# Kernel optimization log

Hardware: AMD Instinct MI355X
Metric: run time of the kernel (lower is better)

The kernel has to match this reference:

```python
import jax, jax.numpy as jnp
import numpy as np

EMB = 768
HEADS = 12
HEAD_DIM = EMB // HEADS


def setup_inputs() -> dict:
    key = jax.random.key(0)
    k1, k2, k3, k4 = jax.random.split(key, 4)
    x = jax.random.normal(k1, (8, 1024, EMB), dtype=jnp.float32)
    # Dense kernels, TF default glorot-ish scale approximated with small normals
    w_qkv = jax.random.normal(k2, (EMB, 3 * EMB), dtype=jnp.float32) * 0.02
    w_out = jax.random.normal(k3, (EMB, EMB), dtype=jnp.float32) * 0.02
    b_out = jnp.zeros((EMB,), dtype=jnp.float32)
    return {"x": x, "w_qkv": w_qkv, "w_out": w_out, "b_out": b_out}


def reference(x, w_qkv, w_out, b_out):
    B, S, E = x.shape
    qkv = jnp.einsum("bse,ef->bsf", x, w_qkv)                 # [B,S,3E]
    qkv = qkv.reshape(B, S, 3, HEADS, HEAD_DIM)
    qkv = jnp.transpose(qkv, (2, 0, 3, 1, 4))                  # [3,B,H,S,D]
    q, k, v = qkv[0], qkv[1], qkv[2]
    scale = jnp.float32(HEAD_DIM) ** -0.5
    # Blocked loop in source computes exact full (non-causal) attention:
    # every query block attends to all keys -> equivalent to standard SDPA.
    scores = jnp.einsum("bhqd,bhkd->bhqk", q, k) * scale       # [B,H,S,S]
    probs = jax.nn.softmax(scores, axis=-1)
    out = jnp.einsum("bhqk,bhkd->bhqd", probs, v)              # [B,H,S,D]
    out = jnp.transpose(out, (0, 2, 1, 3)).reshape(B, S, E)
    return jnp.einsum("bse,ef->bsf", out, w_out) + b_out
```

## Files before the change

kernel.cpp:

```cpp
#include <hip/hip_runtime.h>

typedef float f32x4 __attribute__((ext_vector_type(4)));
typedef short bf16x8 __attribute__((ext_vector_type(8)));

#define MFMA_BF16(a, b, c) __builtin_amdgcn_mfma_f32_16x16x32_bf16((a), (b), (c), 0, 0, 0)

#define GLDS16(gp, lp) __builtin_amdgcn_global_load_lds( \
    (const __attribute__((address_space(1))) unsigned int*)(gp), \
    (__attribute__((address_space(3))) unsigned int*)(lp), 16, 0, 0)

__device__ __forceinline__ ushort f2bf(float f) {
    unsigned int u = __float_as_uint(f);
    return (ushort)((u + 0x7FFFu + ((u >> 16) & 1u)) >> 16);
}

__device__ __forceinline__ float fexp2(float x) {
#if __has_builtin(__builtin_amdgcn_exp2f)
    return __builtin_amdgcn_exp2f(x);
#else
    return exp2f(x);
#endif
}

__global__ __launch_bounds__(256) void prep_kernel(
    const float* __restrict__ x, const float* __restrict__ wq, const float* __restrict__ wo,
    ushort* __restrict__ xb, ushort* __restrict__ wqbt, ushort* __restrict__ wobt)
{
    __shared__ float tile[32][33];
    const int bid = blockIdx.x;
    if (bid < 2048) {
        const float4* src = (const float4*)x;
        ushort4* dst = (ushort4*)xb;
        for (int i = bid * 256 + threadIdx.x; i < 1572864; i += 2048 * 256) {
            float4 v = src[i];
            ushort4 o;
            o.x = f2bf(v.x); o.y = f2bf(v.y); o.z = f2bf(v.z); o.w = f2bf(v.w);
            dst[i] = o;
        }
        return;
    }
    const float* src; ushort* dst; int K, N, bx, by;
    if (bid < 3776) {
        const int L = bid - 2048;
        src = wq; dst = wqbt; K = 768; N = 2304; bx = L % 72; by = L / 72;
    } else {
        const int L = bid - 3776;
        src = wo; dst = wobt; K = 768; N = 768; bx = L % 24; by = L / 24;
    }
    const int n0 = bx * 32, k0 = by * 32;
    const int c = threadIdx.x & 31, rb = threadIdx.x >> 5;
    #pragma unroll
    for (int i = 0; i < 4; ++i)
        tile[i * 8 + rb][c] = src[(size_t)(k0 + i * 8 + rb) * N + n0 + c];
    __syncthreads();
    #pragma unroll
    for (int i = 0; i < 4; ++i) {
        int nr = i * 8 + rb;
        dst[(size_t)(n0 + nr) * K + k0 + c] = f2bf(tile[c][nr]);
    }
}

__global__ __launch_bounds__(256) void gemm_qkv_mfma(
    const ushort* __restrict__ A, const ushort* __restrict__ Bt,
    ushort* __restrict__ Qo, ushort* __restrict__ Ko, ushort* __restrict__ Vo)
{
    __shared__ ushort Al[2][8192];
    __shared__ ushort Bl[2][8192];
    const int tid = threadIdx.x, lane = tid & 63;
    const int wv = tid >> 6, lo = lane & 15, hi = lane >> 4;
    const int wr = wv >> 1, wc = wv & 1;
    const int L = blockIdx.x;
    const int nid = (L & 7) * 144 + (L >> 3);
    const int n0 = (nid % 18) * 128, m0 = (nid / 18) * 128;

    auto stage = [&](int bi, int k0) {
        #pragma unroll
        for (int it = 0; it < 4; ++it) {
            const int p = it * 256 + tid;
            const int row = p >> 3, ch = (p & 7) ^ (row & 7);
            GLDS16(A + (size_t)(m0 + row) * 768 + k0 + ch * 8,
                   &Al[bi][(it * 256 + (tid & 192)) * 8]);
        }
        #pragma unroll
        for (int it = 0; it < 4; ++it) {
            const int p = it * 256 + tid;
            const int row = p >> 3, ch = (p & 7) ^ (row & 7);
            GLDS16(Bt + (size_t)(n0 + row) * 768 + k0 + ch * 8,
                   &Bl[bi][(it * 256 + (tid & 192)) * 8]);
        }
    };

    f32x4 acc[4][4];
    #pragma unroll
    for (int i = 0; i < 4; ++i)
        #pragma unroll
        for (int j = 0; j < 4; ++j)
            acc[i][j] = (f32x4){0.f, 0.f, 0.f, 0.f};

    const int region = n0 / 768;
    const int h = ((n0 % 768) >> 6) + wc;

    stage(0, 0);
    stage(1, 64);

    int cur = 0;
    for (int t = 0; t < 12; ++t) {
        if (t < 11) asm volatile("s_waitcnt vmcnt(8)" ::: "memory");
        else        asm volatile("s_waitcnt vmcnt(0)" ::: "memory");
        __builtin_amdgcn_s_barrier();
        asm volatile("" ::: "memory");

        #pragma unroll
        for (int ks = 0; ks < 2; ++ks) {
            bf16x8 af[4], bfr[4];
            #pragma unroll
            for (int i = 0; i < 4; ++i) {
                const int ra = wr * 64 + i * 16 + lo;
                af[i] = *(const bf16x8*)&Al[cur][ra * 64 + (((ks * 4 + hi) ^ (ra & 7)) * 8)];
                const int rb = wc * 64 + i * 16 + lo;
                bfr[i] = *(const bf16x8*)&Bl[cur][rb * 64 + (((ks * 4 + hi) ^ (rb & 7)) * 8)];
            }
            if (region == 2) {
                #pragma unroll
                for (int mi = 0; mi < 4; ++mi)
                    #pragma unroll
                    for (int nj = 0; nj < 4; ++nj)
                        acc[mi][nj] = MFMA_BF16(af[mi], bfr[nj], acc[mi][nj]);
            } else {
                #pragma unroll
                for (int mi = 0; mi < 4; ++mi)
                    #pragma unroll
                    for (int nj = 0; nj < 4; ++nj)
                        acc[mi][nj] = MFMA_BF16(bfr[nj], af[mi], acc[mi][nj]);
            }
        }

        asm volatile("s_waitcnt lgkmcnt(0)" ::: "memory");
        __builtin_amdgcn_s_barrier();
        asm volatile("" ::: "memory");
        if (t + 2 < 12) stage(cur, (t + 2) * 64);
        cur ^= 1;
    }

    if (region == 2) {
        #pragma unroll
        for (int mi = 0; mi < 4; ++mi) {
            const int m4 = m0 + wr * 64 + mi * 16 + hi * 4;
            const int b = m4 >> 10, s = m4 & 1023;
            #pragma unroll
            for (int nj = 0; nj < 4; ++nj) {
                const int d = nj * 16 + lo;
                ushort4 pk;
                pk.x = f2bf(acc[mi][nj][0]); pk.y = f2bf(acc[mi][nj][1]);
                pk.z = f2bf(acc[mi][nj][2]); pk.w = f2bf(acc[mi][nj][3]);
                *(ushort4*)&Vo[((size_t)(b * 12 + h) * 64 + d) * 1024 + s] = pk;
            }
        }
    } else {
        ushort* dst = region ? Ko : Qo;
        const float sc = region ? 1.0f : 0.18033688011112042f;
        #pragma unroll
        for (int mi = 0; mi < 4; ++mi) {
            const int s_idx = m0 + wr * 64 + mi * 16 + lo;
            const int b = s_idx >> 10, s = s_idx & 1023;
            const size_t base = ((size_t)(b * 12 + h) * 1024 + s) * 64;
            #pragma unroll
            for (int nj = 0; nj < 4; ++nj) {
                ushort4 pk;
                pk.x = f2bf(acc[mi][nj][0] * sc); pk.y = f2bf(acc[mi][nj][1] * sc);
                pk.z = f2bf(acc[mi][nj][2] * sc); pk.w = f2bf(acc[mi][nj][3] * sc);
                *(ushort4*)&dst[base + nj * 16 + hi * 4] = pk;
            }
        }
    }
}

__global__ __launch_bounds__(256) void attn_mfma_kernel(
    const ushort* __restrict__ Qg, const ushort* __restrict__ Kg,
    const ushort* __restrict__ Vg, ushort* __restrict__ AO)
{
    __shared__ ushort Kl[2][4096];
    __shared__ ushort Vl[2][4096];
    __shared__ ushort Pl[4][32 * 72];

    const int tid = threadIdx.x, lane = tid & 63;
    const int wv = tid >> 6, lo = lane & 15, hi = lane >> 4;
    const int L = blockIdx.x;
    const int xcd = L & 7, g = L >> 3;
    const int qb = g / 12;
    const int bh = xcd * 12 + (g % 12);
    const int b = bh / 12, h = bh % 12;
    const size_t kvbase = (size_t)bh * (1024 * 64);

    bf16x8 qa[2][2];
    const int qrow0 = qb * 128 + wv * 32;
    #pragma unroll
    for (int mi = 0; mi < 2; ++mi)
        #pragma unroll
        for (int ks = 0; ks < 2; ++ks)
            qa[mi][ks] = *(const bf16x8*)&Qg[kvbase + (size_t)(qrow0 + mi * 16 + lo) * 64 + ks * 32 + hi * 8];

    f32x4 o[2][4];
    float lp[2] = {0.f, 0.f};
    #pragma unroll
    for (int mi = 0; mi < 2; ++mi)
        #pragma unroll
        for (int dj = 0; dj < 4; ++dj) o[mi][dj] = (f32x4){0.f, 0.f, 0.f, 0.f};

    auto stage = [&](int bi, int kt) {
        #pragma unroll
        for (int it = 0; it < 2; ++it) {
            const int p = it * 256 + tid;
            const int row = p >> 3, ch = (p & 7) ^ (row & 7);
            GLDS16(Kg + kvbase + (size_t)(kt + row) * 64 + ch * 8, &Kl[bi][(it * 256 + (tid & 192)) * 8]);
        }
        #pragma unroll
        for (int it = 0; it < 2; ++it) {
            const int p = it * 256 + tid;
            const int row = p >> 3, ch = (p & 7) ^ (row & 7);
            GLDS16(Vg + kvbase + (size_t)row * 1024 + kt + ch * 8, &Vl[bi][(it * 256 + (tid & 192)) * 8]);
        }
    };

    stage(0, 0);
    __syncthreads();

    for (int t = 0; t < 16; ++t) {
        const int cur = t & 1;
        if (t < 15) stage(cur ^ 1, (t + 1) * 64);

        f32x4 s[2][4];
        #pragma unroll
        for (int mi = 0; mi < 2; ++mi)
            #pragma unroll
            for (int nj = 0; nj < 4; ++nj) s[mi][nj] = (f32x4){0.f, 0.f, 0.f, 0.f};
        #pragma unroll
        for (int ks = 0; ks < 2; ++ks) {
            bf16x8 kb[4];
            #pragma unroll
            for (int nj = 0; nj < 4; ++nj) {
                const int key = nj * 16 + lo, c = ks * 4 + hi;
                kb[nj] = *(const bf16x8*)&Kl[cur][key * 64 + ((c ^ (key & 7)) * 8)];
            }
            #pragma unroll
            for (int mi = 0; mi < 2; ++mi)
                #pragma unroll
                for (int nj = 0; nj < 4; ++nj)
                    s[mi][nj] = MFMA_BF16(kb[nj], qa[mi][ks], s[mi][nj]);
        }

        #pragma unroll
        for (int mi = 0; mi < 2; ++mi) {
            #pragma unroll
            for (int nj = 0; nj < 4; ++nj) {
                const unsigned int u0 = __float_as_uint(fexp2(s[mi][nj][0]));
                const unsigned int u1 = __float_as_uint(fexp2(s[mi][nj][1]));
                const unsigned int u2 = __float_as_uint(fexp2(s[mi][nj][2]));
                const unsigned int u3 = __float_as_uint(fexp2(s[mi][nj][3]));
                const float t0 = __uint_as_float(u0 & 0xFFFF0000u);
                const float t1 = __uint_as_float(u1 & 0xFFFF0000u);
                const float t2 = __uint_as_float(u2 & 0xFFFF0000u);
                const float t3 = __uint_as_float(u3 & 0xFFFF0000u);
                lp[mi] += (t0 + t1) + (t2 + t3);
                ushort4 pk;
                pk.x = (ushort)(u0 >> 16); pk.y = (ushort)(u1 >> 16);
                pk.z = (ushort)(u2 >> 16); pk.w = (ushort)(u3 >> 16);
                *(ushort4*)&Pl[wv][(mi * 16 + lo) * 72 + nj * 16 + hi * 4] = pk;
            }
        }

        #pragma unroll
        for (int ks = 0; ks < 2; ++ks) {
            bf16x8 pa[2];
            #pragma unroll
            for (int mi = 0; mi < 2; ++mi)
                pa[mi] = *(const bf16x8*)&Pl[wv][(mi * 16 + lo) * 72 + ks * 32 + hi * 8];
            bf16x8 vb[4];
            #pragma unroll
            for (int dj = 0; dj < 4; ++dj) {
                const int d = dj * 16 + lo, c = ks * 4 + hi;
                vb[dj] = *(const bf16x8*)&Vl[cur][d * 64 + ((c ^ (d & 7)) * 8)];
            }
            #pragma unroll
            for (int mi = 0; mi < 2; ++mi)
                #pragma unroll
                for (int dj = 0; dj < 4; ++dj)
                    o[mi][dj] = MFMA_BF16(pa[mi], vb[dj], o[mi][dj]);
        }
        __syncthreads();
    }

    #pragma unroll
    for (int mi = 0; mi < 2; ++mi) {
        float l = lp[mi];
        l += __shfl_xor(l, 16);
        l += __shfl_xor(l, 32);
        #pragma unroll
        for (int r = 0; r < 4; ++r) {
            const float lr = __shfl(l, hi * 4 + r, 16);
            const float rcp = 1.0f / lr;
            const int srow = qrow0 + mi * 16 + hi * 4 + r;
            #pragma unroll
            for (int dj = 0; dj < 4; ++dj)
                AO[((size_t)(b * 1024 + srow)) * 768 + h * 64 + dj * 16 + lo] =
                    f2bf(o[mi][dj][r] * rcp);
        }
    }
}

__global__ __launch_bounds__(256) void gemm_out_mfma(
    const ushort* __restrict__ A, const ushort* __restrict__ Bt,
    const float* __restrict__ bias, float* __restrict__ C)
{
    __shared__ ushort Al[2][8192];
    __shared__ ushort Bl[2][8192];
    const int tid = threadIdx.x, lane = tid & 63;
    const int wv = tid >> 6, lo = lane & 15, hi = lane >> 4;
    const int wr = wv >> 1, wc = wv & 1;
    const int L = blockIdx.x;
    const int nid = (L & 7) * 48 + (L >> 3);
    const int n0 = (nid % 6) * 128, m0 = (nid / 6) * 128;

    auto stage = [&](int bi, int k0) {
        #pragma unroll
        for (int it = 0; it < 4; ++it) {
            const int p = it * 256 + tid;
            const int row = p >> 3, ch = (p & 7) ^ (row & 7);
            GLDS16(A + (size_t)(m0 + row) * 768 + k0 + ch * 8,
                   &Al[bi][(it * 256 + (tid & 192)) * 8]);
        }
        #pragma unroll
        for (int it = 0; it < 4; ++it) {
            const int p = it * 256 + tid;
            const int row = p >> 3, ch = (p & 7) ^ (row & 7);
            GLDS16(Bt + (size_t)(n0 + row) * 768 + k0 + ch * 8,
                   &Bl[bi][(it * 256 + (tid & 192)) * 8]);
        }
    };

    f32x4 acc[4][4];
    #pragma unroll
    for (int i = 0; i < 4; ++i)
        #pragma unroll
        for (int j = 0; j < 4; ++j)
            acc[i][j] = (f32x4){0.f, 0.f, 0.f, 0.f};

    stage(0, 0);
    stage(1, 64);

    int cur = 0;
    for (int t = 0; t < 12; ++t) {
        if (t < 11) asm volatile("s_waitcnt vmcnt(8)" ::: "memory");
        else        asm volatile("s_waitcnt vmcnt(0)" ::: "memory");
        __builtin_amdgcn_s_barrier();
        asm volatile("" ::: "memory");

        #pragma unroll
        for (int ks = 0; ks < 2; ++ks) {
            bf16x8 af[4], bfr[4];
            #pragma unroll
            for (int i = 0; i < 4; ++i) {
                const int ra = wr * 64 + i * 16 + lo;
                af[i] = *(const bf16x8*)&Al[cur][ra * 64 + (((ks * 4 + hi) ^ (ra & 7)) * 8)];
                const int rb = wc * 64 + i * 16 + lo;
                bfr[i] = *(const bf16x8*)&Bl[cur][rb * 64 + (((ks * 4 + hi) ^ (rb & 7)) * 8)];
            }
            #pragma unroll
            for (int mi = 0; mi < 4; ++mi)
                #pragma unroll
                for (int nj = 0; nj < 4; ++nj)
                    acc[mi][nj] = MFMA_BF16(bfr[nj], af[mi], acc[mi][nj]);
        }

        asm volatile("s_waitcnt lgkmcnt(0)" ::: "memory");
        __builtin_amdgcn_s_barrier();
        asm volatile("" ::: "memory");
        if (t + 2 < 12) stage(cur, (t + 2) * 64);
        cur ^= 1;
    }

    const int ncol0 = n0 + wc * 64;
    #pragma unroll
    for (int mi = 0; mi < 4; ++mi) {
        const int m = m0 + wr * 64 + mi * 16 + lo;
        #pragma unroll
        for (int nj = 0; nj < 4; ++nj) {
            const int nb = ncol0 + nj * 16 + hi * 4;
            const float4 bv = *reinterpret_cast<const float4*>(&bias[nb]);
            float4 ov;
            ov.x = acc[mi][nj][0] + bv.x; ov.y = acc[mi][nj][1] + bv.y;
            ov.z = acc[mi][nj][2] + bv.z; ov.w = acc[mi][nj][3] + bv.w;
            *reinterpret_cast<float4*>(&C[(size_t)m * 768 + nb]) = ov;
        }
    }
}

extern "C" void kernel_launch(void* const* d_in, const int* in_sizes, int n_in,
                              void* d_out, int out_size, void* d_ws, size_t ws_size,
                              hipStream_t stream) {
    const float* x     = (const float*)d_in[0];
    const float* w_qkv = (const float*)d_in[1];
    const float* w_out = (const float*)d_in[2];
    const float* b_out = (const float*)d_in[3];
    float* out = (float*)d_out;

    (void)in_sizes; (void)n_in; (void)out_size; (void)ws_size;

    ushort* xb   = (ushort*)d_ws;
    ushort* wqbt = xb + 6291456;
    ushort* wobt = wqbt + 1769472;
    ushort* Qs   = wobt + 589824;
    ushort* Ks   = Qs + 6291456;
    ushort* Vt   = Ks + 6291456;
    ushort* AO   = Vt + 6291456;

    prep_kernel<<<4352, 256, 0, stream>>>(x, w_qkv, w_out, xb, wqbt, wobt);
    gemm_qkv_mfma<<<1152, 256, 0, stream>>>(xb, wqbt, Qs, Ks, Vt);
    attn_mfma_kernel<<<768, 256, 0, stream>>>(Qs, Ks, Vt, AO);
    gemm_out_mfma<<<384, 256, 0, stream>>>(AO, wobt, b_out, out);
}
```

Measured before the change: 122.9 us.

## Fuse x fp32-to-bf16 conversion into QKV GEMM loads and raise MFMA priority

The separate pass that converts x to bf16 is removed. The QKV GEMM now streams fp32 x tiles straight into LDS and converts them to bf16 in registers with packed cvt instructions. To keep the LDS footprint the same, the K-tile is halved to 32, so there are twice as many pipeline iterations and barriers. The attention kernel also wraps its MFMA blocks in s_setprio so matrix work is favoured over other waves. This saves writing and re-reading a 12MB intermediate, but doubles the fp32 A traffic into LDS and adds barrier overhead.

```diff
diff --git a/kernel.cpp b/kernel.cpp
--- a/kernel.cpp
+++ b/kernel.cpp
@@ -22,29 +22,26 @@
 #endif
 }
 
+__device__ __forceinline__ bf16x8 cvt8(f32x4 a, f32x4 b) {
+    union { bf16x8 v; unsigned int u[4]; } r;
+    asm("v_cvt_pk_bf16_f32 %0, %1, %2" : "=v"(r.u[0]) : "v"(a[0]), "v"(a[1]));
+    asm("v_cvt_pk_bf16_f32 %0, %1, %2" : "=v"(r.u[1]) : "v"(a[2]), "v"(a[3]));
+    asm("v_cvt_pk_bf16_f32 %0, %1, %2" : "=v"(r.u[2]) : "v"(b[0]), "v"(b[1]));
+    asm("v_cvt_pk_bf16_f32 %0, %1, %2" : "=v"(r.u[3]) : "v"(b[2]), "v"(b[3]));
+    return r.v;
+}
+
 __global__ __launch_bounds__(256) void prep_kernel(
-    const float* __restrict__ x, const float* __restrict__ wq, const float* __restrict__ wo,
-    ushort* __restrict__ xb, ushort* __restrict__ wqbt, ushort* __restrict__ wobt)
+    const float* __restrict__ wq, const float* __restrict__ wo,
+    ushort* __restrict__ wqbt, ushort* __restrict__ wobt)
 {
     __shared__ float tile[32][33];
     const int bid = blockIdx.x;
-    if (bid < 2048) {
-        const float4* src = (const float4*)x;
-        ushort4* dst = (ushort4*)xb;
-        for (int i = bid * 256 + threadIdx.x; i < 1572864; i += 2048 * 256) {
-            float4 v = src[i];
-            ushort4 o;
-            o.x = f2bf(v.x); o.y = f2bf(v.y); o.z = f2bf(v.z); o.w = f2bf(v.w);
-            dst[i] = o;
-        }
-        return;
-    }
     const float* src; ushort* dst; int K, N, bx, by;
-    if (bid < 3776) {
-        const int L = bid - 2048;
-        src = wq; dst = wqbt; K = 768; N = 2304; bx = L % 72; by = L / 72;
+    if (bid < 1728) {
+        src = wq; dst = wqbt; K = 768; N = 2304; bx = bid % 72; by = bid / 72;
     } else {
-        const int L = bid - 3776;
+        const int L = bid - 1728;
         src = wo; dst = wobt; K = 768; N = 768; bx = L % 24; by = L / 24;
     }
     const int n0 = bx * 32, k0 = by * 32;
@@ -61,11 +58,11 @@
 }
 
 __global__ __launch_bounds__(256) void gemm_qkv_mfma(
-    const ushort* __restrict__ A, const ushort* __restrict__ Bt,
+    const float* __restrict__ X, const ushort* __restrict__ Bt,
     ushort* __restrict__ Qo, ushort* __restrict__ Ko, ushort* __restrict__ Vo)
 {
-    __shared__ ushort Al[2][8192];
-    __shared__ ushort Bl[2][8192];
+    __shared__ float  Af[2][4096];
+    __shared__ ushort Bl[2][4096];
     const int tid = threadIdx.x, lane = tid & 63;
     const int wv = tid >> 6, lo = lane & 15, hi = lane >> 4;
     const int wr = wv >> 1, wc = wv & 1;
@@ -76,16 +73,16 @@
     auto stage = [&](int bi, int k0) {
         #pragma unroll
         for (int it = 0; it < 4; ++it) {
-            const int p = it * 256 + tid;
-            const int row = p >> 3, ch = (p & 7) ^ (row & 7);
-            GLDS16(A + (size_t)(m0 + row) * 768 + k0 + ch * 8,
-                   &Al[bi][(it * 256 + (tid & 192)) * 8]);
-        }
-        #pragma unroll
-        for (int it = 0; it < 4; ++it) {
-            const int p = it * 256 + tid;
-            const int row = p >> 3, ch = (p & 7) ^ (row & 7);
-            GLDS16(Bt + (size_t)(n0 + row) * 768 + k0 + ch * 8,
+            const int q = it * 256 + tid;
+            const int row = q >> 3, c = q & 7;
+            GLDS16(X + (size_t)(m0 + row) * 768 + k0 + ((c ^ (row & 7)) * 4),
+                   &Af[bi][(it * 256 + (tid & 192)) * 4]);
+        }
+        #pragma unroll
+        for (int it = 0; it < 2; ++it) {
+            const int q = it * 256 + tid;
+            const int row = q >> 2, c = q & 3;
+            GLDS16(Bt + (size_t)(n0 + row) * 768 + k0 + ((c ^ (row & 3)) * 8),
                    &Bl[bi][(it * 256 + (tid & 192)) * 8]);
         }
     };
@@ -101,44 +98,43 @@
     const int h = ((n0 % 768) >> 6) + wc;
 
     stage(0, 0);
-    stage(1, 64);
+    stage(1, 32);
 
     int cur = 0;
-    for (int t = 0; t < 12; ++t) {
-        if (t < 11) asm volatile("s_waitcnt vmcnt(8)" ::: "memory");
+    for (int t = 0; t < 24; ++t) {
+        if (t < 23) asm volatile("s_waitcnt vmcnt(6)" ::: "memory");
         else        asm volatile("s_waitcnt vmcnt(0)" ::: "memory");
         __builtin_amdgcn_s_barrier();
         asm volatile("" ::: "memory");
 
-        #pragma unroll
-        for (int ks = 0; ks < 2; ++ks) {
-            bf16x8 af[4], bfr[4];
-            #pragma unroll
-            for (int i = 0; i < 4; ++i) {
-                const int ra = wr * 64 + i * 16 + lo;
-                af[i] = *(const bf16x8*)&Al[cur][ra * 64 + (((ks * 4 + hi) ^ (ra & 7)) * 8)];
-                const int rb = wc * 64 + i * 16 + lo;
-                bfr[i] = *(const bf16x8*)&Bl[cur][rb * 64 + (((ks * 4 + hi) ^ (rb & 7)) * 8)];
-            }
-            if (region == 2) {
+        bf16x8 af[4], bfr[4];
+        #pragma unroll
+        for (int i = 0; i < 4; ++i) {
+            const int ra = wr * 64 + i * 16 + lo;
+            const f32x4 a0 = *(const f32x4*)&Af[cur][ra * 32 + (((2 * hi)     ^ (ra & 7)) * 4)];
+            const f32x4 a1 = *(const f32x4*)&Af[cur][ra * 32 + (((2 * hi + 1) ^ (ra & 7)) * 4)];
+            af[i] = cvt8(a0, a1);
+            const int rb = wc * 64 + i * 16 + lo;
+            bfr[i] = *(const bf16x8*)&Bl[cur][rb * 32 + ((hi ^ (rb & 3)) * 8)];
+        }
+        if (region == 2) {
+            #pragma unroll
+            for (int mi = 0; mi < 4; ++mi)
                 #pragma unroll
-                for (int mi = 0; mi < 4; ++mi)
-                    #pragma unroll
-                    for (int nj = 0; nj < 4; ++nj)
-                        acc[mi][nj] = MFMA_BF16(af[mi], bfr[nj], acc[mi][nj]);
-            } else {
+                for (int nj = 0; nj < 4; ++nj)
+                    acc[mi][nj] = MFMA_BF16(af[mi], bfr[nj], acc[mi][nj]);
+        } else {
+            #pragma unroll
+            for (int mi = 0; mi < 4; ++mi)
                 #pragma unroll
-                for (int mi = 0; mi < 4; ++mi)
-                    #pragma unroll
-                    for (int nj = 0; nj < 4; ++nj)
-                        acc[mi][nj] = MFMA_BF16(bfr[nj], af[mi], acc[mi][nj]);
-            }
+                for (int nj = 0; nj < 4; ++nj)
+                    acc[mi][nj] = MFMA_BF16(bfr[nj], af[mi], acc[mi][nj]);
         }
 
         asm volatile("s_waitcnt lgkmcnt(0)" ::: "memory");
         __builtin_amdgcn_s_barrier();
         asm volatile("" ::: "memory");
-        if (t + 2 < 12) stage(cur, (t + 2) * 64);
+        if (t + 2 < 24) stage(cur, (t + 2) * 32);
         cur ^= 1;
     }
 
@@ -242,11 +238,13 @@
                 const int key = nj * 16 + lo, c = ks * 4 + hi;
                 kb[nj] = *(const bf16x8*)&Kl[cur][key * 64 + ((c ^ (key & 7)) * 8)];
             }
+            __builtin_amdgcn_s_setprio(1);
             #pragma unroll
             for (int mi = 0; mi < 2; ++mi)
                 #pragma unroll
                 for (int nj = 0; nj < 4; ++nj)
                     s[mi][nj] = MFMA_BF16(kb[nj], qa[mi][ks], s[mi][nj]);
+            __builtin_amdgcn_s_setprio(0);
         }
 
         #pragma unroll
@@ -281,11 +279,13 @@
                 const int d = dj * 16 + lo, c = ks * 4 + hi;
                 vb[dj] = *(const bf16x8*)&Vl[cur][d * 64 + ((c ^ (d & 7)) * 8)];
             }
+            __builtin_amdgcn_s_setprio(1);
             #pragma unroll
             for (int mi = 0; mi < 2; ++mi)
                 #pragma unroll
                 for (int dj = 0; dj < 4; ++dj)
                     o[mi][dj] = MFMA_BF16(pa[mi], vb[dj], o[mi][dj]);
+            __builtin_amdgcn_s_setprio(0);
         }
         __syncthreads();
     }
@@ -406,16 +406,15 @@
 
     (void)in_sizes; (void)n_in; (void)out_size; (void)ws_size;
 
-    ushort* xb   = (ushort*)d_ws;
-    ushort* wqbt = xb + 6291456;
+    ushort* wqbt = (ushort*)d_ws;
     ushort* wobt = wqbt + 1769472;
     ushort* Qs   = wobt + 589824;
     ushort* Ks   = Qs + 6291456;
     ushort* Vt   = Ks + 6291456;
     ushort* AO   = Vt + 6291456;
 
-    prep_kernel<<<4352, 256, 0, stream>>>(x, w_qkv, w_out, xb, wqbt, wobt);
-    gemm_qkv_mfma<<<1152, 256, 0, stream>>>(xb, wqbt, Qs, Ks, Vt);
+    prep_kernel<<<2304, 256, 0, stream>>>(w_qkv, w_out, wqbt, wobt);
+    gemm_qkv_mfma<<<1152, 256, 0, stream>>>(x, wqbt, Qs, Ks, Vt);
     attn_mfma_kernel<<<768, 256, 0, stream>>>(Qs, Ks, Vt, AO);
     gemm_out_mfma<<<384, 256, 0, stream>>>(AO, wobt, b_out, out);
 }
```

Measured after the change: 139.1 us. 1.13x slower.

## Enlarge QKV GEMM tiles to 256x256 with 8 waves and staggered staging

Applied to the files above, without the earlier changes.

The QKV projection GEMM now uses 256x256 output tiles computed by 512-thread blocks (8 waves, 2x4 layout). Each wave holds a 128x64 accumulator, and the grid drops from 1152 to 288 blocks. Loads are interleaved in quarter-steps with barriers, B fragments are kept in registers per K-tile, and s_setprio raises MFMA priority. The attention kernel also gets s_setprio around its MFMA loops. The aim is higher data reuse and better overlap of loads with compute. The cost is more registers and LDS per block and fewer blocks, with 288 blocks on 256 CUs leaving a partial second wave.

```diff
diff --git a/kernel.cpp b/kernel.cpp
--- a/kernel.cpp
+++ b/kernel.cpp
@@ -60,92 +60,168 @@
     }
 }
 
-__global__ __launch_bounds__(256) void gemm_qkv_mfma(
+__global__ __launch_bounds__(512, 2) void gemm_qkv_mfma(
     const ushort* __restrict__ A, const ushort* __restrict__ Bt,
     ushort* __restrict__ Qo, ushort* __restrict__ Ko, ushort* __restrict__ Vo)
 {
-    __shared__ ushort Al[2][8192];
-    __shared__ ushort Bl[2][8192];
+    __shared__ ushort Abuf[2][16384];
+    __shared__ ushort Bbuf[2][16384];
     const int tid = threadIdx.x, lane = tid & 63;
     const int wv = tid >> 6, lo = lane & 15, hi = lane >> 4;
-    const int wr = wv >> 1, wc = wv & 1;
+    const int wr = wv >> 2, wc = wv & 3;
     const int L = blockIdx.x;
-    const int nid = (L & 7) * 144 + (L >> 3);
-    const int n0 = (nid % 18) * 128, m0 = (nid / 18) * 128;
-
-    auto stage = [&](int bi, int k0) {
-        #pragma unroll
-        for (int it = 0; it < 4; ++it) {
-            const int p = it * 256 + tid;
-            const int row = p >> 3, ch = (p & 7) ^ (row & 7);
-            GLDS16(A + (size_t)(m0 + row) * 768 + k0 + ch * 8,
-                   &Al[bi][(it * 256 + (tid & 192)) * 8]);
-        }
-        #pragma unroll
-        for (int it = 0; it < 4; ++it) {
-            const int p = it * 256 + tid;
-            const int row = p >> 3, ch = (p & 7) ^ (row & 7);
-            GLDS16(Bt + (size_t)(n0 + row) * 768 + k0 + ch * 8,
-                   &Bl[bi][(it * 256 + (tid & 192)) * 8]);
+    const int nid = (L & 7) * 36 + (L >> 3);
+    const int m0 = (nid / 9) * 256, n0 = (nid % 9) * 256;
+
+    const int region = n0 / 768;
+
+    auto stageA = [&](int bi, int half, int kt) {
+        #pragma unroll
+        for (int c = 0; c < 2; ++c) {
+            const int cl = c * 512 + tid;
+            const int row = half * 128 + (cl >> 3), sl = cl & 7;
+            GLDS16(A + (size_t)(m0 + row) * 768 + kt * 64 + ((sl ^ (row & 7)) * 8),
+                   &Abuf[bi][(half * 1024 + c * 512 + (tid & 448)) * 8]);
         }
     };
-
-    f32x4 acc[4][4];
-    #pragma unroll
-    for (int i = 0; i < 4; ++i)
+    auto stageB = [&](int bi, int half, int kt) {
+        #pragma unroll
+        for (int c = 0; c < 2; ++c) {
+            const int cl = c * 512 + tid;
+            const int row = half * 128 + (cl >> 3), sl = cl & 7;
+            GLDS16(Bt + (size_t)(n0 + row) * 768 + kt * 64 + ((sl ^ (row & 7)) * 8),
+                   &Bbuf[bi][(half * 1024 + c * 512 + (tid & 448)) * 8]);
+        }
+    };
+
+    f32x4 acc[8][4];
+    #pragma unroll
+    for (int i = 0; i < 8; ++i)
         #pragma unroll
         for (int j = 0; j < 4; ++j)
             acc[i][j] = (f32x4){0.f, 0.f, 0.f, 0.f};
 
-    const int region = n0 / 768;
-    const int h = ((n0 % 768) >> 6) + wc;
-
-    stage(0, 0);
-    stage(1, 64);
-
-    int cur = 0;
-    for (int t = 0; t < 12; ++t) {
-        if (t < 11) asm volatile("s_waitcnt vmcnt(8)" ::: "memory");
-        else        asm volatile("s_waitcnt vmcnt(0)" ::: "memory");
-        __builtin_amdgcn_s_barrier();
-        asm volatile("" ::: "memory");
-
-        #pragma unroll
-        for (int ks = 0; ks < 2; ++ks) {
-            bf16x8 af[4], bfr[4];
-            #pragma unroll
-            for (int i = 0; i < 4; ++i) {
-                const int ra = wr * 64 + i * 16 + lo;
-                af[i] = *(const bf16x8*)&Al[cur][ra * 64 + (((ks * 4 + hi) ^ (ra & 7)) * 8)];
-                const int rb = wc * 64 + i * 16 + lo;
-                bfr[i] = *(const bf16x8*)&Bl[cur][rb * 64 + (((ks * 4 + hi) ^ (rb & 7)) * 8)];
-            }
+    stageB(0, 0, 0); stageB(0, 1, 0);
+    stageA(0, 0, 0); stageA(0, 1, 0);
+    stageB(1, 0, 1); stageB(1, 1, 1);
+    asm volatile("s_waitcnt vmcnt(4)" ::: "memory");
+    __builtin_amdgcn_s_barrier();
+    asm volatile("" ::: "memory");
+
+    bf16x8 bfr[8];
+
+    for (int it = 0; it < 6; ++it) {
+        const int t1 = 2 * it + 1;
+        const int kB2 = (2 * it + 2) % 12;
+        const int kB3 = (2 * it + 3) % 12;
+
+        #pragma unroll
+        for (int q = 0; q < 4; ++q) {
+            if (q == 0) {
+                #pragma unroll
+                for (int nj = 0; nj < 4; ++nj)
+                    #pragma unroll
+                    for (int ks = 0; ks < 2; ++ks) {
+                        const int row = wc * 64 + nj * 16 + lo;
+                        bfr[nj * 2 + ks] = *(const bf16x8*)&Bbuf[0][row * 64 + (((ks * 4 + hi) ^ (row & 7)) * 8)];
+                    }
+            }
+            bf16x8 af[4];
+            #pragma unroll
+            for (int mm = 0; mm < 2; ++mm)
+                #pragma unroll
+                for (int ks = 0; ks < 2; ++ks) {
+                    const int row = wr * 128 + (2 * q + mm) * 16 + lo;
+                    af[mm * 2 + ks] = *(const bf16x8*)&Abuf[0][row * 64 + (((ks * 4 + hi) ^ (row & 7)) * 8)];
+                }
+            if (q == 0)      stageA(1, 0, t1);
+            else if (q == 1) stageA(1, 1, t1);
+            else if (q == 2) stageB(0, 0, kB2);
+            else             stageB(0, 1, kB2);
+            if (q == 0) asm volatile("s_waitcnt lgkmcnt(8)" ::: "memory");
+            __builtin_amdgcn_s_barrier();
+            asm volatile("s_waitcnt lgkmcnt(0)" ::: "memory");
+            __builtin_amdgcn_s_setprio(1);
             if (region == 2) {
                 #pragma unroll
-                for (int mi = 0; mi < 4; ++mi)
+                for (int mm = 0; mm < 2; ++mm)
                     #pragma unroll
                     for (int nj = 0; nj < 4; ++nj)
-                        acc[mi][nj] = MFMA_BF16(af[mi], bfr[nj], acc[mi][nj]);
+                        #pragma unroll
+                        for (int ks = 0; ks < 2; ++ks)
+                            acc[2 * q + mm][nj] = MFMA_BF16(af[mm * 2 + ks], bfr[nj * 2 + ks], acc[2 * q + mm][nj]);
             } else {
                 #pragma unroll
-                for (int mi = 0; mi < 4; ++mi)
+                for (int mm = 0; mm < 2; ++mm)
                     #pragma unroll
                     for (int nj = 0; nj < 4; ++nj)
-                        acc[mi][nj] = MFMA_BF16(bfr[nj], af[mi], acc[mi][nj]);
-            }
-        }
-
-        asm volatile("s_waitcnt lgkmcnt(0)" ::: "memory");
-        __builtin_amdgcn_s_barrier();
-        asm volatile("" ::: "memory");
-        if (t + 2 < 12) stage(cur, (t + 2) * 64);
-        cur ^= 1;
-    }
-
+                        #pragma unroll
+                        for (int ks = 0; ks < 2; ++ks)
+                            acc[2 * q + mm][nj] = MFMA_BF16(bfr[nj * 2 + ks], af[mm * 2 + ks], acc[2 * q + mm][nj]);
+            }
+            __builtin_amdgcn_s_setprio(0);
+            if (q == 3) asm volatile("s_waitcnt vmcnt(4)" ::: "memory");
+            __builtin_amdgcn_s_barrier();
+            asm volatile("" ::: "memory");
+        }
+
+        #pragma unroll
+        for (int q = 0; q < 4; ++q) {
+            if (q == 0) {
+                #pragma unroll
+                for (int nj = 0; nj < 4; ++nj)
+                    #pragma unroll
+                    for (int ks = 0; ks < 2; ++ks) {
+                        const int row = wc * 64 + nj * 16 + lo;
+                        bfr[nj * 2 + ks] = *(const bf16x8*)&Bbuf[1][row * 64 + (((ks * 4 + hi) ^ (row & 7)) * 8)];
+                    }
+            }
+            bf16x8 af[4];
+            #pragma unroll
+            for (int mm = 0; mm < 2; ++mm)
+                #pragma unroll
+                for (int ks = 0; ks < 2; ++ks) {
+                    const int row = wr * 128 + (2 * q + mm) * 16 + lo;
+                    af[mm * 2 + ks] = *(const bf16x8*)&Abuf[1][row * 64 + (((ks * 4 + hi) ^ (row & 7)) * 8)];
+                }
+            if (q == 0)      stageA(0, 0, kB2);
+            else if (q == 1) stageA(0, 1, kB2);
+            else if (q == 2) stageB(1, 0, kB3);
+            else             stageB(1, 1, kB3);
+            if (q == 0) asm volatile("s_waitcnt lgkmcnt(8)" ::: "memory");
+            __builtin_amdgcn_s_barrier();
+            asm volatile("s_waitcnt lgkmcnt(0)" ::: "memory");
+            __builtin_amdgcn_s_setprio(1);
+            if (region == 2) {
+                #pragma unroll
+                for (int mm = 0; mm < 2; ++mm)
+                    #pragma unroll
+                    for (int nj = 0; nj < 4; ++nj)
+                        #pragma unroll
+                        for (int ks = 0; ks < 2; ++ks)
+                            acc[2 * q + mm][nj] = MFMA_BF16(af[mm * 2 + ks], bfr[nj * 2 + ks], acc[2 * q + mm][nj]);
+            } else {
+                #pragma unroll
+                for (int mm = 0; mm < 2; ++mm)
+                    #pragma unroll
+                    for (int nj = 0; nj < 4; ++nj)
+                        #pragma unroll
+                        for (int ks = 0; ks < 2; ++ks)
+                            acc[2 * q + mm][nj] = MFMA_BF16(bfr[nj * 2 + ks], af[mm * 2 + ks], acc[2 * q + mm][nj]);
+            }
+            __builtin_amdgcn_s_setprio(0);
+            if (q == 3) asm volatile("s_waitcnt vmcnt(4)" ::: "memory");
+            __builtin_amdgcn_s_barrier();
+            asm volatile("" ::: "memory");
+        }
+    }
+    asm volatile("s_waitcnt vmcnt(0)" ::: "memory");
+
+    const int h = ((n0 + wc * 64) % 768) >> 6;
     if (region == 2) {
         #pragma unroll
-        for (int mi = 0; mi < 4; ++mi) {
-            const int m4 = m0 + wr * 64 + mi * 16 + hi * 4;
+        for (int mi = 0; mi < 8; ++mi) {
+            const int m4 = m0 + wr * 128 + mi * 16 + hi * 4;
             const int b = m4 >> 10, s = m4 & 1023;
             #pragma unroll
             for (int nj = 0; nj < 4; ++nj) {
@@ -160,8 +236,8 @@
         ushort* dst = region ? Ko : Qo;
         const float sc = region ? 1.0f : 0.18033688011112042f;
         #pragma unroll
-        for (int mi = 0; mi < 4; ++mi) {
-            const int s_idx = m0 + wr * 64 + mi * 16 + lo;
+        for (int mi = 0; mi < 8; ++mi) {
+            const int s_idx = m0 + wr * 128 + mi * 16 + lo;
             const int b = s_idx >> 10, s = s_idx & 1023;
             const size_t base = ((size_t)(b * 12 + h) * 1024 + s) * 64;
             #pragma unroll
@@ -242,11 +318,13 @@
                 const int key = nj * 16 + lo, c = ks * 4 + hi;
                 kb[nj] = *(const bf16x8*)&Kl[cur][key * 64 + ((c ^ (key & 7)) * 8)];
             }
+            __builtin_amdgcn_s_setprio(1);
             #pragma unroll
             for (int mi = 0; mi < 2; ++mi)
                 #pragma unroll
                 for (int nj = 0; nj < 4; ++nj)
                     s[mi][nj] = MFMA_BF16(kb[nj], qa[mi][ks], s[mi][nj]);
+            __builtin_amdgcn_s_setprio(0);
         }
 
         #pragma unroll
@@ -281,11 +359,13 @@
                 const int d = dj * 16 + lo, c = ks * 4 + hi;
                 vb[dj] = *(const bf16x8*)&Vl[cur][d * 64 + ((c ^ (d & 7)) * 8)];
             }
+            __builtin_amdgcn_s_setprio(1);
             #pragma unroll
             for (int mi = 0; mi < 2; ++mi)
                 #pragma unroll
                 for (int dj = 0; dj < 4; ++dj)
                     o[mi][dj] = MFMA_BF16(pa[mi], vb[dj], o[mi][dj]);
+            __builtin_amdgcn_s_setprio(0);
         }
         __syncthreads();
     }
@@ -415,7 +495,7 @@
     ushort* AO   = Vt + 6291456;
 
     prep_kernel<<<4352, 256, 0, stream>>>(x, w_qkv, w_out, xb, wqbt, wobt);
-    gemm_qkv_mfma<<<1152, 256, 0, stream>>>(xb, wqbt, Qs, Ks, Vt);
+    gemm_qkv_mfma<<<288, 512, 0, stream>>>(xb, wqbt, Qs, Ks, Vt);
     attn_mfma_kernel<<<768, 256, 0, stream>>>(Qs, Ks, Vt, AO);
     gemm_out_mfma<<<384, 256, 0, stream>>>(AO, wobt, b_out, out);
 }
```

Result: slower. 186.8 us (+52.1%).

## Make QKV GEMM persistent over three N-tiles per block; raise MFMA wave priority

Applied to the files above, without the earlier changes.

The QKV projection GEMM now launches 384 blocks, each handling three consecutive 128-column N-tiles for one M-tile. It streams 36 K-stages through a single continuous double-buffered pipeline and writes each tile's output when that tile finishes, instead of launching 1152 one-tile blocks. This removes the per-block prologue and tail, keeps the prefetch running across tile boundaries, and reuses the A rows that stay hot in cache. In exchange there is less parallelism (384 blocks against the CU count) and the epilogue stores now sit inside the loop. Separately, the attention kernel wraps its MFMA sequences in s_setprio so waves issuing matrix ops get scheduling priority.

```diff
diff --git a/kernel.cpp b/kernel.cpp
--- a/kernel.cpp
+++ b/kernel.cpp
@@ -70,10 +70,14 @@
     const int wv = tid >> 6, lo = lane & 15, hi = lane >> 4;
     const int wr = wv >> 1, wc = wv & 1;
     const int L = blockIdx.x;
-    const int nid = (L & 7) * 144 + (L >> 3);
-    const int n0 = (nid % 18) * 128, m0 = (nid / 18) * 128;
-
-    auto stage = [&](int bi, int k0) {
+    const int nid = (L & 7) * 48 + (L >> 3);
+    const int m0 = (nid / 6) * 128;
+    const int ngrp = nid % 6;
+    const int region = ngrp >> 1;
+
+    auto stage = [&](int bi, int s) {
+        const int k0 = (s % 12) * 64;
+        const int n0 = (ngrp * 3 + s / 12) * 128;
         #pragma unroll
         for (int it = 0; it < 4; ++it) {
             const int p = it * 256 + tid;
@@ -97,15 +101,12 @@
         for (int j = 0; j < 4; ++j)
             acc[i][j] = (f32x4){0.f, 0.f, 0.f, 0.f};
 
-    const int region = n0 / 768;
-    const int h = ((n0 % 768) >> 6) + wc;
-
     stage(0, 0);
-    stage(1, 64);
+    stage(1, 1);
 
     int cur = 0;
-    for (int t = 0; t < 12; ++t) {
-        if (t < 11) asm volatile("s_waitcnt vmcnt(8)" ::: "memory");
+    for (int s = 0; s < 36; ++s) {
+        if (s < 35) asm volatile("s_waitcnt vmcnt(8)" ::: "memory");
         else        asm volatile("s_waitcnt vmcnt(0)" ::: "memory");
         __builtin_amdgcn_s_barrier();
         asm volatile("" ::: "memory");
@@ -138,40 +139,50 @@
         asm volatile("s_waitcnt lgkmcnt(0)" ::: "memory");
         __builtin_amdgcn_s_barrier();
         asm volatile("" ::: "memory");
-        if (t + 2 < 12) stage(cur, (t + 2) * 64);
+
+        if ((s % 12) == 11) {
+            const int n0g = (ngrp * 3 + s / 12) * 128;
+            const int h = ((n0g % 768) >> 6) + wc;
+            if (region == 2) {
+                #pragma unroll
+                for (int mi = 0; mi < 4; ++mi) {
+                    const int m4 = m0 + wr * 64 + mi * 16 + hi * 4;
+                    const int b = m4 >> 10, sx = m4 & 1023;
+                    #pragma unroll
+                    for (int nj = 0; nj < 4; ++nj) {
+                        const int d = nj * 16 + lo;
+                        ushort4 pk;
+                        pk.x = f2bf(acc[mi][nj][0]); pk.y = f2bf(acc[mi][nj][1]);
+                        pk.z = f2bf(acc[mi][nj][2]); pk.w = f2bf(acc[mi][nj][3]);
+                        *(ushort4*)&Vo[((size_t)(b * 12 + h) * 64 + d) * 1024 + sx] = pk;
+                    }
+                }
+            } else {
+                ushort* dst = region ? Ko : Qo;
+                const float sc = region ? 1.0f : 0.18033688011112042f;
+                #pragma unroll
+                for (int mi = 0; mi < 4; ++mi) {
+                    const int s_idx = m0 + wr * 64 + mi * 16 + lo;
+                    const int b = s_idx >> 10, sx = s_idx & 1023;
+                    const size_t base = ((size_t)(b * 12 + h) * 1024 + sx) * 64;
+                    #pragma unroll
+                    for (int nj = 0; nj < 4; ++nj) {
+                        ushort4 pk;
+                        pk.x = f2bf(acc[mi][nj][0] * sc); pk.y = f2bf(acc[mi][nj][1] * sc);
+                        pk.z = f2bf(acc[mi][nj][2] * sc); pk.w = f2bf(acc[mi][nj][3] * sc);
+                        *(ushort4*)&dst[base + nj * 16 + hi * 4] = pk;
+                    }
+                }
+            }
+            #pragma unroll
+            for (int i = 0; i < 4; ++i)
+                #pragma unroll
+                for (int j = 0; j < 4; ++j)
+                    acc[i][j] = (f32x4){0.f, 0.f, 0.f, 0.f};
+        }
+
+        if (s + 2 < 36) stage(cur, s + 2);
         cur ^= 1;
-    }
-
-    if (region == 2) {
-        #pragma unroll
-        for (int mi = 0; mi < 4; ++mi) {
-            const int m4 = m0 + wr * 64 + mi * 16 + hi * 4;
-            const int b = m4 >> 10, s = m4 & 1023;
-            #pragma unroll
-            for (int nj = 0; nj < 4; ++nj) {
-                const int d = nj * 16 + lo;
-                ushort4 pk;
-                pk.x = f2bf(acc[mi][nj][0]); pk.y = f2bf(acc[mi][nj][1]);
-                pk.z = f2bf(acc[mi][nj][2]); pk.w = f2bf(acc[mi][nj][3]);
-                *(ushort4*)&Vo[((size_t)(b * 12 + h) * 64 + d) * 1024 + s] = pk;
-            }
-        }
-    } else {
-        ushort* dst = region ? Ko : Qo;
-        const float sc = region ? 1.0f : 0.18033688011112042f;
-        #pragma unroll
-        for (int mi = 0; mi < 4; ++mi) {
-            const int s_idx = m0 + wr * 64 + mi * 16 + lo;
-            const int b = s_idx >> 10, s = s_idx & 1023;
-            const size_t base = ((size_t)(b * 12 + h) * 1024 + s) * 64;
-            #pragma unroll
-            for (int nj = 0; nj < 4; ++nj) {
-                ushort4 pk;
-                pk.x = f2bf(acc[mi][nj][0] * sc); pk.y = f2bf(acc[mi][nj][1] * sc);
-                pk.z = f2bf(acc[mi][nj][2] * sc); pk.w = f2bf(acc[mi][nj][3] * sc);
-                *(ushort4*)&dst[base + nj * 16 + hi * 4] = pk;
-            }
-        }
     }
 }
 
@@ -242,11 +253,13 @@
                 const int key = nj * 16 + lo, c = ks * 4 + hi;
                 kb[nj] = *(const bf16x8*)&Kl[cur][key * 64 + ((c ^ (key & 7)) * 8)];
             }
+            __builtin_amdgcn_s_setprio(1);
             #pragma unroll
             for (int mi = 0; mi < 2; ++mi)
                 #pragma unroll
                 for (int nj = 0; nj < 4; ++nj)
                     s[mi][nj] = MFMA_BF16(kb[nj], qa[mi][ks], s[mi][nj]);
+            __builtin_amdgcn_s_setprio(0);
         }
 
         #pragma unroll
@@ -281,11 +294,13 @@
                 const int d = dj * 16 + lo, c = ks * 4 + hi;
                 vb[dj] = *(const bf16x8*)&Vl[cur][d * 64 + ((c ^ (d & 7)) * 8)];
             }
+            __builtin_amdgcn_s_setprio(1);
             #pragma unroll
             for (int mi = 0; mi < 2; ++mi)
                 #pragma unroll
                 for (int dj = 0; dj < 4; ++dj)
                     o[mi][dj] = MFMA_BF16(pa[mi], vb[dj], o[mi][dj]);
+            __builtin_amdgcn_s_setprio(0);
         }
         __syncthreads();
     }
@@ -415,7 +430,7 @@
     ushort* AO   = Vt + 6291456;
 
     prep_kernel<<<4352, 256, 0, stream>>>(x, w_qkv, w_out, xb, wqbt, wobt);
-    gemm_qkv_mfma<<<1152, 256, 0, stream>>>(xb, wqbt, Qs, Ks, Vt);
+    gemm_qkv_mfma<<<384, 256, 0, stream>>>(xb, wqbt, Qs, Ks, Vt);
     attn_mfma_kernel<<<768, 256, 0, stream>>>(Qs, Ks, Vt, AO);
     gemm_out_mfma<<<384, 256, 0, stream>>>(AO, wobt, b_out, out);
 }
```

Result: slower. 163.6 us (+33.2%).
